# Performance work log

Measured on AMD Instinct MI355X. Metric: run time of the kernel, lower is better.

## Reference

```python
import jax, jax.numpy as jnp
import numpy as np

N_QUBITS = 4  # kernel 2x2 -> 4 pixels -> 4 qubits -> 4 PauliZ outputs
KH, KW = 2, 2
STRIDE = 2
OUT_CHANNELS = 4


def _cnot(state, c, t):
    # state: [P, 2,2,2,2]; qubit q lives on axis q+1
    ca, ta = c + 1, t + 1
    s0 = jax.lax.index_in_dim(state, 0, ca, keepdims=True)
    s1 = jnp.flip(jax.lax.index_in_dim(state, 1, ca, keepdims=True), axis=ta)
    return jnp.concatenate([s0, s1], axis=ca)


def _ry(state, theta_q, q):
    c, s = jnp.cos(theta_q / 2), jnp.sin(theta_q / 2)
    M = jnp.stack([jnp.stack([c, -s]), jnp.stack([s, c])])  # [2,2] real RY
    out = jnp.tensordot(M, state, axes=([1], [q + 1]))
    return jnp.moveaxis(out, 0, q + 1)


def _qnode(angles, theta):
    # angles: [P, 4] patch pixels used as RY embedding angles
    c, s = jnp.cos(angles / 2), jnp.sin(angles / 2)
    # product state |psi> = RY(a0)|0> x RY(a1)|0> x RY(a2)|0> x RY(a3)|0>
    state = jnp.einsum('pa,pb,pc,pd->pabcd',
                       jnp.stack([c[:, 0], s[:, 0]], -1),
                       jnp.stack([c[:, 1], s[:, 1]], -1),
                       jnp.stack([c[:, 2], s[:, 2]], -1),
                       jnp.stack([c[:, 3], s[:, 3]], -1))
    for q in range(N_QUBITS):            # entangling CNOT ring
        state = _cnot(state, q, (q + 1) % N_QUBITS)
    for q in range(N_QUBITS):            # trainable RY layer
        state = _ry(state, theta[q], q)
    p = state * state                    # real amplitudes -> probabilities
    outs = []
    for q in range(N_QUBITS):            # <Z_q> expectation values
        axes = tuple(a for a in range(1, N_QUBITS + 1) if a != q + 1)
        m = jnp.sum(p, axis=axes)        # [P, 2]
        outs.append(m[:, 0] - m[:, 1])
    return jnp.stack(outs, axis=-1)      # [P, 4]


def _quanv(xc, theta, out_per):
    # xc: [B, 1, H, W]; stride == kernel so unfold == blocked reshape
    B, _, H, W = xc.shape
    Ho, Wo = (H - KH) // STRIDE + 1, (W - KW) // STRIDE + 1
    # unfold ordering: patch pixels row-major (di*KW+dj), patches row-major over (Ho,Wo)
    patches = xc.reshape(B, Ho, KH, Wo, KW).transpose(0, 1, 3, 2, 4).reshape(B, Ho * Wo, KH * KW)
    # torch.stack over unbound patch dim puts L (patches) outermost: [L, B, 4]
    patches = patches.transpose(1, 0, 2).reshape(-1, KH * KW)  # [L*B, 4]
    vals = _qnode(patches, theta)                              # [L*B, 4]
    # faithful to the original raw .view of the contiguous [L, B, 4] buffer
    return vals.reshape(B, out_per, Ho, Wo)


def reference(x, theta):
    B, C, H, W = x.shape
    out_per = OUT_CHANNELS // C
    outs = [_quanv(x[:, c:c + 1], theta, out_per) for c in range(C)]
    return jnp.concatenate(outs, axis=1)


def setup_inputs() -> dict:
    key = jax.random.key(0)
    k1, k2 = jax.random.split(key)
    x = jax.random.normal(k1, (32, 1, 512, 512), dtype=jnp.float32)
    theta = jax.random.normal(k2, (4,), dtype=jnp.float32)
    return {"x": x, "theta": theta}
```

## Files before the change

kernel.cpp:

```cpp
#include <hip/hip_runtime.h>

#define HH 512
#define WW 512
#define HO 256
#define WO 256
#define LTOT (HO * WO)

#define INV_2PI 0.15915494309189535f

__global__ __launch_bounds__(256) void quanv_kernel(const float* __restrict__ x,
                                                    const float* __restrict__ theta,
                                                    float* __restrict__ out) {
    __shared__ float4 lds[1024];

    const int tid   = threadIdx.x;
    const int l0    = blockIdx.x * 32;
    const int irow  = l0 >> 8;
    const int j0    = l0 & 255;
    const int lpair = tid & 15;
    const int b0    = tid >> 4;

    float ct[4], st[4];
#pragma unroll
    for (int q = 0; q < 4; ++q) {
        const float r = theta[q] * INV_2PI;
        st[q] = __builtin_amdgcn_sinf(r);
        ct[q] = __builtin_amdgcn_cosf(r);
    }

    const int col  = 2 * (j0 + 2 * lpair);
    const int off0 = (2 * irow) * WW + col;
    const int off1 = off0 + WW;

    const float* xb0 = x + (size_t)b0 * (HH * WW);
    const float* xb1 = x + (size_t)(b0 + 16) * (HH * WW);
    const float4 r0a = *(const float4*)(xb0 + off0);
    const float4 r1a = *(const float4*)(xb0 + off1);
    const float4 r0b = *(const float4*)(xb1 + off0);
    const float4 r1b = *(const float4*)(xb1 + off1);

#pragma unroll
    for (int w = 0; w < 2; ++w) {
        const int b = b0 + 16 * w;
        const float4 r0 = w ? r0b : r0a;
        const float4 r1 = w ? r1b : r1a;
#pragma unroll
        for (int c = 0; c < 2; ++c) {
            const float aa[4] = {c ? r0.z : r0.x, c ? r0.w : r0.y,
                                 c ? r1.z : r1.x, c ? r1.w : r1.y};
            float ca[4], sa[4];
#pragma unroll
            for (int k = 0; k < 4; ++k) {
                const float r = aa[k] * INV_2PI;
                sa[k] = __builtin_amdgcn_sinf(r);
                ca[k] = __builtin_amdgcn_cosf(r);
            }
            const float A1 = ca[0] * ca[1];
            const float A2 = A1 * ca[2];
            const float A3 = A2 * ca[3];
            const float A0 = (ca[1] * ca[2]) * ca[3];
            const float B0 = sa[0] * sa[1];
            const float B1 = sa[1] * sa[2];
            const float B2 = sa[2] * sa[3];
            const float B3 = B0 * sa[3];
            const float z0 = ct[0] * A0 - st[0] * B0;
            const float z1 = ct[1] * A1 - st[1] * B1;
            const float z2 = ct[2] * A2 - st[2] * B2;
            const float z3 = ct[3] * A3 - st[3] * B3;

            const int lsub = 2 * lpair + c;
            lds[lsub * 32 + (b ^ (lsub & 31))] = make_float4(z0, z1, z2, z3);
        }
    }

    __syncthreads();

    float4* out4 = (float4*)out + (size_t)l0 * 32;
#pragma unroll
    for (int k = 0; k < 4; ++k) {
        const int idx = k * 256 + tid;
        const int ls = idx >> 5, bb = idx & 31;
        out4[idx] = lds[ls * 32 + (bb ^ (ls & 31))];
    }
}

extern "C" void kernel_launch(void* const* d_in, const int* in_sizes, int n_in,
                              void* d_out, int out_size, void* d_ws, size_t ws_size,
                              hipStream_t stream) {
    const float* x     = (const float*)d_in[0];
    const float* theta = (const float*)d_in[1];
    float* out         = (float*)d_out;

    const int blocks = LTOT / 32;
    quanv_kernel<<<blocks, 256, 0, stream>>>(x, theta, out);
}
```

Baseline: 80.92 us.

## Process two patch tiles per block with double-buffered LDS and nontemporal stores

```diff
diff --git a/kernel.cpp b/kernel.cpp
--- a/kernel.cpp
+++ b/kernel.cpp
@@ -8,13 +8,41 @@
 
 #define INV_2PI 0.15915494309189535f
 
+typedef float f4 __attribute__((ext_vector_type(4)));
+
+__device__ __forceinline__ f4 qnode(float a0, float a1, float a2, float a3,
+                                    const float* __restrict__ ct,
+                                    const float* __restrict__ st) {
+    float ca[4], sa[4];
+    const float r0 = a0 * INV_2PI, r1 = a1 * INV_2PI, r2 = a2 * INV_2PI, r3 = a3 * INV_2PI;
+    sa[0] = __builtin_amdgcn_sinf(r0); ca[0] = __builtin_amdgcn_cosf(r0);
+    sa[1] = __builtin_amdgcn_sinf(r1); ca[1] = __builtin_amdgcn_cosf(r1);
+    sa[2] = __builtin_amdgcn_sinf(r2); ca[2] = __builtin_amdgcn_cosf(r2);
+    sa[3] = __builtin_amdgcn_sinf(r3); ca[3] = __builtin_amdgcn_cosf(r3);
+    const float A1 = ca[0] * ca[1];
+    const float A2 = A1 * ca[2];
+    const float A3 = A2 * ca[3];
+    const float A0 = (ca[1] * ca[2]) * ca[3];
+    const float B0 = sa[0] * sa[1];
+    const float B1 = sa[1] * sa[2];
+    const float B2 = sa[2] * sa[3];
+    const float B3 = B0 * sa[3];
+    f4 z;
+    z.x = ct[0] * A0 - st[0] * B0;
+    z.y = ct[1] * A1 - st[1] * B1;
+    z.z = ct[2] * A2 - st[2] * B2;
+    z.w = ct[3] * A3 - st[3] * B3;
+    return z;
+}
+
 __global__ __launch_bounds__(256) void quanv_kernel(const float* __restrict__ x,
                                                     const float* __restrict__ theta,
                                                     float* __restrict__ out) {
-    __shared__ float4 lds[1024];
+    __shared__ f4 ldsA[1024];
+    __shared__ f4 ldsB[1024];
 
     const int tid   = threadIdx.x;
-    const int l0    = blockIdx.x * 32;
+    const int l0    = blockIdx.x * 64;
     const int irow  = l0 >> 8;
     const int j0    = l0 & 255;
     const int lpair = tid & 15;
@@ -28,59 +56,70 @@
         ct[q] = __builtin_amdgcn_cosf(r);
     }
 
-    const int col  = 2 * (j0 + 2 * lpair);
-    const int off0 = (2 * irow) * WW + col;
-    const int off1 = off0 + WW;
-
+    const int colT0 = 2 * (j0 + 2 * lpair);
+    const int colT1 = colT0 + 64;
+    const int r0off = (2 * irow) * WW;
+    const int r1off = r0off + WW;
     const float* xb0 = x + (size_t)b0 * (HH * WW);
     const float* xb1 = x + (size_t)(b0 + 16) * (HH * WW);
-    const float4 r0a = *(const float4*)(xb0 + off0);
-    const float4 r1a = *(const float4*)(xb0 + off1);
-    const float4 r0b = *(const float4*)(xb1 + off0);
-    const float4 r1b = *(const float4*)(xb1 + off1);
+
+    const f4 t0r0a = *(const f4*)(xb0 + r0off + colT0);
+    const f4 t0r1a = *(const f4*)(xb0 + r1off + colT0);
+    const f4 t0r0b = *(const f4*)(xb1 + r0off + colT0);
+    const f4 t0r1b = *(const f4*)(xb1 + r1off + colT0);
+    const f4 t1r0a = *(const f4*)(xb0 + r0off + colT1);
+    const f4 t1r1a = *(const f4*)(xb0 + r1off + colT1);
+    const f4 t1r0b = *(const f4*)(xb1 + r0off + colT1);
+    const f4 t1r1b = *(const f4*)(xb1 + r1off + colT1);
 
 #pragma unroll
     for (int w = 0; w < 2; ++w) {
         const int b = b0 + 16 * w;
-        const float4 r0 = w ? r0b : r0a;
-        const float4 r1 = w ? r1b : r1a;
+        const f4 r0 = w ? t0r0b : t0r0a;
+        const f4 r1 = w ? t0r1b : t0r1a;
 #pragma unroll
         for (int c = 0; c < 2; ++c) {
-            const float aa[4] = {c ? r0.z : r0.x, c ? r0.w : r0.y,
-                                 c ? r1.z : r1.x, c ? r1.w : r1.y};
-            float ca[4], sa[4];
+            const f4 z = qnode(c ? r0.z : r0.x, c ? r0.w : r0.y,
+                               c ? r1.z : r1.x, c ? r1.w : r1.y, ct, st);
+            const int lsub = 2 * lpair + c;
+            ldsA[lsub * 32 + (b ^ (lsub & 31))] = z;
+        }
+    }
+    __syncthreads();
+
+    {
+        f4* o = (f4*)out + (size_t)l0 * 32;
 #pragma unroll
-            for (int k = 0; k < 4; ++k) {
-                const float r = aa[k] * INV_2PI;
-                sa[k] = __builtin_amdgcn_sinf(r);
-                ca[k] = __builtin_amdgcn_cosf(r);
-            }
-            const float A1 = ca[0] * ca[1];
-            const float A2 = A1 * ca[2];
-            const float A3 = A2 * ca[3];
-            const float A0 = (ca[1] * ca[2]) * ca[3];
-            const float B0 = sa[0] * sa[1];
-            const float B1 = sa[1] * sa[2];
-            const float B2 = sa[2] * sa[3];
-            const float B3 = B0 * sa[3];
-            const float z0 = ct[0] * A0 - st[0] * B0;
-            const float z1 = ct[1] * A1 - st[1] * B1;
-            const float z2 = ct[2] * A2 - st[2] * B2;
-            const float z3 = ct[3] * A3 - st[3] * B3;
-
-            const int lsub = 2 * lpair + c;
-            lds[lsub * 32 + (b ^ (lsub & 31))] = make_float4(z0, z1, z2, z3);
+        for (int k = 0; k < 4; ++k) {
+            const int idx = k * 256 + tid;
+            const int ls = idx >> 5, bb = idx & 31;
+            __builtin_nontemporal_store(ldsA[ls * 32 + (bb ^ (ls & 31))], &o[idx]);
         }
     }
 
+#pragma unroll
+    for (int w = 0; w < 2; ++w) {
+        const int b = b0 + 16 * w;
+        const f4 r0 = w ? t1r0b : t1r0a;
+        const f4 r1 = w ? t1r1b : t1r1a;
+#pragma unroll
+        for (int c = 0; c < 2; ++c) {
+            const f4 z = qnode(c ? r0.z : r0.x, c ? r0.w : r0.y,
+                               c ? r1.z : r1.x, c ? r1.w : r1.y, ct, st);
+            const int lsub = 2 * lpair + c;
+            ldsB[lsub * 32 + (b ^ (lsub & 31))] = z;
+        }
+    }
     __syncthreads();
 
-    float4* out4 = (float4*)out + (size_t)l0 * 32;
+    {
+        f4* o = (f4*)out + (size_t)(l0 + 32) * 32;
 #pragma unroll
-    for (int k = 0; k < 4; ++k) {
-        const int idx = k * 256 + tid;
-        const int ls = idx >> 5, bb = idx & 31;
-        out4[idx] = lds[ls * 32 + (bb ^ (ls & 31))];
+        for (int k = 0; k < 4; ++k) {
+            const int idx = k * 256 + tid;
+            const int ls = idx >> 5, bb = idx & 31;
+            __builtin_nontemporal_store(ldsB[ls * 32 + (bb ^ (ls & 31))], &o[idx]);
+        }
     }
 }
 
@@ -91,6 +130,6 @@
     const float* theta = (const float*)d_in[1];
     float* out         = (float*)d_out;
 
-    const int blocks = LTOT / 32;
+    const int blocks = LTOT / 64;
     quanv_kernel<<<blocks, 256, 0, stream>>>(x, theta, out);
 }
```

Measured after the change: 81.00 us. Within noise of the previous version (+0.1%).
